# Kernel tuning notes

Hardware: AMD Instinct MI355X
Metric: run time of the kernel (lower is better)

The kernel has to match this reference:

```python
import jax, jax.numpy as jnp
import numpy as np

G = 17  # groups == deform_groups
EPS = 1e-5

# regular 3x3 kernel grid in homogeneous coords: rows = (dy, dx, 1), cols = 9 kernel taps (row-major)
REG = jnp.array([[-1, -1, -1, 0, 0, 0, 1, 1, 1],
                 [-1, 0, 1, -1, 0, 1, -1, 0, 1],
                 [1, 1, 1, 1, 1, 1, 1, 1, 1]], dtype=jnp.float32)
KY = jnp.array([-1, -1, -1, 0, 0, 0, 1, 1, 1], dtype=jnp.float32)
KX = jnp.array([-1, 0, 1, -1, 0, 1, -1, 0, 1], dtype=jnp.float32)


def setup_inputs() -> dict:
    key = jax.random.key(0)
    k0, k1, k2 = jax.random.split(key, 3)
    B, C, H, W = 2, 272, 128, 128
    Cg = C // G
    x = jax.random.normal(k0, (B, C, H, W), jnp.float32)
    tm_w = jax.random.normal(k1, (6 * G, Cg, 3, 3), jnp.float32) * 0.02  # offset-transform conv weight
    tm_b = jnp.zeros((6 * G,), jnp.float32)
    dc_w = jax.random.normal(k2, (C, Cg, 3, 3), jnp.float32) * 0.05     # deform conv weight (no bias)
    gamma = jnp.ones((C,), jnp.float32)
    beta = jnp.zeros((C,), jnp.float32)
    return dict(x=x, tm_w=tm_w, tm_b=tm_b, dc_w=dc_w, gamma=gamma, beta=beta)


def _deform_sample(x, dy, dx):
    """Bilinear-sample x (B,C,H,W) at per-group offsets dy,dx (B,H,W,G,9).
    Returns (B,G,Cg,9,H,W). Zero padding outside the image (mmcv semantics)."""
    B, C, H, W = x.shape
    Cg = C // G
    hh = jnp.arange(H, dtype=x.dtype)[None, :, None, None, None]
    ww = jnp.arange(W, dtype=x.dtype)[None, None, :, None, None]
    py = hh + KY + dy  # (B,H,W,G,9)
    px = ww + KX + dx
    y0 = jnp.floor(py)
    x0 = jnp.floor(px)
    wy = py - y0
    wx = px - x0
    y0i = y0.astype(jnp.int32)
    x0i = x0.astype(jnp.int32)
    x_g = x.reshape(B, G, Cg, H * W)

    def corner(yi, xi, wgt):
        valid = (yi >= 0) & (yi < H) & (xi >= 0) & (xi < W)
        lin = jnp.clip(yi, 0, H - 1) * W + jnp.clip(xi, 0, W - 1)  # (B,H,W,G,9)
        lin = lin.transpose(0, 3, 4, 1, 2).reshape(B, G, 1, 9 * H * W)
        idx = jnp.broadcast_to(lin, (B, G, Cg, 9 * H * W))
        vals = jnp.take_along_axis(x_g, idx, axis=3).reshape(B, G, Cg, 9, H, W)
        w = (wgt * valid.astype(x.dtype)).transpose(0, 3, 4, 1, 2)  # (B,G,9,H,W)
        return vals * w[:, :, None]

    samp = corner(y0i, x0i, (1 - wy) * (1 - wx))
    samp = samp + corner(y0i, x0i + 1, (1 - wy) * wx)
    samp = samp + corner(y0i + 1, x0i, wy * (1 - wx))
    samp = samp + corner(y0i + 1, x0i + 1, wy * wx)
    return samp


def _forward(x, tm_w, tm_b, dc_w, gamma, beta):
    B, C, H, W = x.shape
    Cg = C // G
    # 1) offset-transform conv (grouped 3x3, SAME)
    aff = jax.lax.conv_general_dilated(
        x, tm_w, window_strides=(1, 1), padding='SAME',
        dimension_numbers=('NCHW', 'OIHW', 'NCHW'), feature_group_count=G)
    aff = aff + tm_b[None, :, None, None]  # (B,6G,H,W)
    # faithful to torch: view(B,2,3,G,H,W).permute(0,4,5,3,1,2) @ REG
    aff = aff.reshape(B, 2, 3, G, H, W).transpose(0, 4, 5, 3, 1, 2)  # (B,H,W,G,2,3)
    off = jnp.einsum('bhwgij,jk->bhwgik', aff, REG)  # (B,H,W,G,2,9)
    # DeformConv2d reads the flattened 18 channels as interleaved (dy,dx) pairs per tap
    off = off.reshape(B, H, W, G, 18).reshape(B, H, W, G, 9, 2)
    dy, dx = off[..., 0], off[..., 1]
    # 2) deformable 3x3 conv, groups=deform_groups=G, bias=False
    samp = _deform_sample(x, dy, dx)  # (B,G,Cg,9,H,W)
    w = dc_w.reshape(G, Cg, Cg, 3 * 3)  # (g, out-in-group, in-in-group, tap)
    out = jnp.einsum('bgckhw,gock->bgohw', samp, w).reshape(B, C, H, W)
    # 3) batch norm (training-mode stats) + residual ReLU
    mean = jnp.mean(out, axis=(0, 2, 3), keepdims=True)
    var = jnp.var(out, axis=(0, 2, 3), keepdims=True)
    out = (out - mean) * jax.lax.rsqrt(var + EPS)
    out = out * gamma[None, :, None, None] + beta[None, :, None, None]
    return jax.nn.relu(out + x)


def reference(x, tm_w, tm_b, dc_w, gamma, beta):
    return _forward(x, tm_w, tm_b, dc_w, gamma, beta)
```

## Files before the change

kernel.cpp:

```cpp
#include <hip/hip_runtime.h>
#include <math.h>

#define BB 2
#define CC 272
#define GG 17
#define CG 16
#define HH 128
#define WW 128
#define HWX (HH*WW)
#define AFFC 102
#define NSLAB (BB*GG)
#define TILES_PER_SLAB 128
#define NWG (NSLAB*TILES_PER_SLAB)
#define WGPX (NWG/8)
#define PSTR ((size_t)NSLAB*HWX*4)

typedef float f4nt __attribute__((ext_vector_type(4)));
typedef float f2nt __attribute__((ext_vector_type(2)));
typedef unsigned u4nt __attribute__((ext_vector_type(4)));
typedef _Float16 h2 __attribute__((ext_vector_type(2)));

__device__ __forceinline__ h2 bch(unsigned u) { return __builtin_bit_cast(h2, u); }
__device__ __forceinline__ unsigned hpk(float a, float b) {
    return __builtin_bit_cast(unsigned, __builtin_amdgcn_cvt_pkrtz(a, b));
}
__device__ __forceinline__ h2 hbc(float a) {
    return __builtin_bit_cast(h2, __builtin_amdgcn_cvt_pkrtz(a, a));
}

#if __has_builtin(__builtin_amdgcn_fdot2)
#define FDOT2(A, B, C) __builtin_amdgcn_fdot2((A), (B), (C), false)
#else
#define FDOT2(A, B, C) fmaf((float)(A).x, (float)(B).x, fmaf((float)(A).y, (float)(B).y, (C)))
#endif

__device__ __forceinline__ unsigned f2bf(float f) {
    unsigned u = __float_as_uint(f);
    return (u + 0x7fffu + ((u >> 16) & 1u)) >> 16;
}
__device__ __forceinline__ float bflo(unsigned u) { return __uint_as_float(u << 16); }
__device__ __forceinline__ float bfhi(unsigned u) { return __uint_as_float(u & 0xffff0000u); }

__global__ __launch_bounds__(256) void wt_kernel(
    const float* __restrict__ dc_w, const float* __restrict__ tm_w,
    unsigned* __restrict__ dc_wh, unsigned* __restrict__ tm_wh)
{
    int i = blockIdx.x * 256 + threadIdx.x;
    if (i < GG * 8 * 9 * CG) {
        int oc = i & 15, t = (i >> 4) % 9, cp = (i / 144) % 8, g = i / 1152;
        float w0 = dc_w[((size_t)(g * 16 + oc) * 16 + 2 * cp) * 9 + t];
        float w1 = dc_w[((size_t)(g * 16 + oc) * 16 + 2 * cp + 1) * 9 + t];
        dc_wh[i] = hpk(w0, w1);
    }
    if (i < GG * 6 * 9 * 8) {
        int cp = i & 7, t = (i >> 3) % 9, j = (i / 72) % 6, ig = i / 432;
        float w0 = tm_w[((size_t)(ig * 6 + j) * 16 + 2 * cp) * 9 + t];
        float w1 = tm_w[((size_t)(ig * 6 + j) * 16 + 2 * cp + 1) * 9 + t];
        tm_wh[i] = hpk(w0, w1);
    }
}

__global__ __launch_bounds__(256) void transpose_kernel(
    const float* __restrict__ x, unsigned* __restrict__ xt)
{
    __shared__ float tile[CG][WW + 1];
    const int h = blockIdx.x & (HH - 1);
    const int g = (blockIdx.x >> 7) % GG;
    const int b = blockIdx.x / (GG * HH);
    const int tid = threadIdx.x;
    const float* src = x + (size_t)(b * CC + g * CG) * HWX + h * WW;
    for (int i = tid; i < CG * WW; i += 256) {
        int c = i >> 7, w = i & (WW - 1);
        tile[c][w] = src[(size_t)c * HWX + w];
    }
    __syncthreads();
    const size_t rowbase = ((size_t)(b * GG + g) * HWX + h * WW) * 4;
    unsigned* d0 = xt + rowbase;
    unsigned* d1 = xt + PSTR + rowbase;
    for (int i = tid; i < 4 * WW; i += 256) {
        int w = i >> 2, c4 = i & 3;
        d0[(size_t)w * 4 + c4] = hpk(tile[2 * c4][w],     tile[2 * c4 + 1][w]);
        d1[(size_t)w * 4 + c4] = hpk(tile[8 + 2 * c4][w], tile[8 + 2 * c4 + 1][w]);
    }
}

__global__ __launch_bounds__(128) void aff_conv_kernel(
    const unsigned* __restrict__ xt, const unsigned* __restrict__ tm_wh,
    const float* __restrict__ tm_b, float* __restrict__ aff2)
{
    const int ig = blockIdx.y;
    const int b = blockIdx.z;
    const int tid = threadIdx.x;

    const int p = blockIdx.x * 128 + tid;
    const int h = p >> 7, w = p & (WW - 1);
    const unsigned* xb0 = xt + (size_t)(b * GG + ig) * HWX * 4;
    const unsigned* xb1 = xb0 + PSTR;
    const unsigned* wbh = tm_wh + (size_t)ig * (6 * 9 * 8);

    float acc[6];
#pragma unroll
    for (int j = 0; j < 6; ++j) acc[j] = 0.f;

#pragma unroll 1
    for (int t = 0; t < 9; ++t) {
        int hy = h + t / 3 - 1;
        int wx = w + t % 3 - 1;
        uint4 u0 = {0, 0, 0, 0}, u1 = {0, 0, 0, 0};
        if (hy >= 0 && hy < HH && wx >= 0 && wx < WW) {
            u0 = *(const uint4*)(xb0 + (size_t)(hy * WW + wx) * 4);
            u1 = *(const uint4*)(xb1 + (size_t)(hy * WW + wx) * 4);
        }
#pragma unroll
        for (int j = 0; j < 6; ++j) {
            const uint4* wp = (const uint4*)(wbh + (j * 9 + t) * 8);
            uint4 qa = wp[0], qb = wp[1];
            float a = acc[j];
            a = FDOT2(bch(u0.x), bch(qa.x), a); a = FDOT2(bch(u0.y), bch(qa.y), a);
            a = FDOT2(bch(u0.z), bch(qa.z), a); a = FDOT2(bch(u0.w), bch(qa.w), a);
            a = FDOT2(bch(u1.x), bch(qb.x), a); a = FDOT2(bch(u1.y), bch(qb.y), a);
            a = FDOT2(bch(u1.z), bch(qb.z), a); a = FDOT2(bch(u1.w), bch(qb.w), a);
            acc[j] = a;
        }
    }
#pragma unroll
    for (int j = 0; j < 6; ++j) {
        int o = ig * 6 + j;
        int i_ = o / 51, rem = o % 51;
        int j2 = rem / 17, gp = rem % 17;
        int e = i_ * 3 + j2;
        aff2[((size_t)(b * GG + gp) * HWX + p) * 6 + e] = acc[j] + tm_b[o];
    }
}


#define MACC(T, CP, S2) { \
    const uint4* wp_ = (const uint4*)(wgh + ((CP) * 9 + (T)) * CG); \
    uint4 q0 = wp_[0], q1 = wp_[1], q2 = wp_[2], q3 = wp_[3]; \
    acc[0]  = FDOT2(S2, bch(q0.x), acc[0]);  acc[1]  = FDOT2(S2, bch(q0.y), acc[1]); \
    acc[2]  = FDOT2(S2, bch(q0.z), acc[2]);  acc[3]  = FDOT2(S2, bch(q0.w), acc[3]); \
    acc[4]  = FDOT2(S2, bch(q1.x), acc[4]);  acc[5]  = FDOT2(S2, bch(q1.y), acc[5]); \
    acc[6]  = FDOT2(S2, bch(q1.z), acc[6]);  acc[7]  = FDOT2(S2, bch(q1.w), acc[7]); \
    acc[8]  = FDOT2(S2, bch(q2.x), acc[8]);  acc[9]  = FDOT2(S2, bch(q2.y), acc[9]); \
    acc[10] = FDOT2(S2, bch(q2.z), acc[10]); acc[11] = FDOT2(S2, bch(q2.w), acc[11]); \
    acc[12] = FDOT2(S2, bch(q3.x), acc[12]); acc[13] = FDOT2(S2, bch(q3.y), acc[13]); \
    acc[14] = FDOT2(S2, bch(q3.z), acc[14]); acc[15] = FDOT2(S2, bch(q3.w), acc[15]); }

#define SEM(T, CP, UA, UB, UC, UD) { \
    h2 s2 = bch(UA) * W00 + bch(UB) * W01 + bch(UC) * W10 + bch(UD) * W11; \
    MACC(T, CP, s2) }

#define TAP(T, I0, K0, I1, K1) { \
    float dy = ((I0) ? a10 : a00) * (float)((K0) / 3 - 1) \
             + ((I0) ? a11 : a01) * (float)((K0) % 3 - 1) + ((I0) ? a12 : a02); \
    float dx = ((I1) ? a10 : a00) * (float)((K1) / 3 - 1) \
             + ((I1) ? a11 : a01) * (float)((K1) % 3 - 1) + ((I1) ? a12 : a02); \
    float py = (float)(h + (T) / 3 - 1) + dy; \
    float px = (float)(w + (T) % 3 - 1) + dx; \
    float y0f = floorf(py), x0f = floorf(px); \
    float wy = py - y0f, wx = px - x0f; \
    int y0 = (int)y0f, x0 = (int)x0f; \
    int y1 = y0 + 1, x1 = x0 + 1; \
    bool vy0 = (y0 >= 0) && (y0 < HH), vy1 = (y1 >= 0) && (y1 < HH); \
    bool vx0 = (x0 >= 0) && (x0 < WW), vx1 = (x1 >= 0) && (x1 < WW); \
    int y0c = min(max(y0, 0), HH - 1), y1c = min(max(y1, 0), HH - 1); \
    int x0c = min(max(x0, 0), WW - 1), x1c = min(max(x1, 0), WW - 1); \
    float w00 = (vy0 && vx0) ? (1.f - wy) * (1.f - wx) : 0.f; \
    float w01 = (vy0 && vx1) ? (1.f - wy) * wx : 0.f; \
    float w10 = (vy1 && vx0) ? wy * (1.f - wx) : 0.f; \
    float w11 = (vy1 && vx1) ? wy * wx : 0.f; \
    h2 W00 = hbc(w00), W01 = hbc(w01), W10 = hbc(w10), W11 = hbc(w11); \
    int l00 = y0c * WW + x0c, l01 = y0c * WW + x1c; \
    int l10 = y1c * WW + x0c, l11 = y1c * WW + x1c; \
    uint4 A0 = *(const uint4*)(xb0 + (size_t)l00 * 4); \
    uint4 A1 = *(const uint4*)(xb1 + (size_t)l00 * 4); \
    uint4 B0 = *(const uint4*)(xb0 + (size_t)l01 * 4); \
    uint4 B1 = *(const uint4*)(xb1 + (size_t)l01 * 4); \
    uint4 C0 = *(const uint4*)(xb0 + (size_t)l10 * 4); \
    uint4 C1 = *(const uint4*)(xb1 + (size_t)l10 * 4); \
    uint4 D0 = *(const uint4*)(xb0 + (size_t)l11 * 4); \
    uint4 D1 = *(const uint4*)(xb1 + (size_t)l11 * 4); \
    SEM(T, 0, A0.x, B0.x, C0.x, D0.x) SEM(T, 1, A0.y, B0.y, C0.y, D0.y) \
    SEM(T, 2, A0.z, B0.z, C0.z, D0.z) SEM(T, 3, A0.w, B0.w, C0.w, D0.w) \
    SEM(T, 4, A1.x, B1.x, C1.x, D1.x) SEM(T, 5, A1.y, B1.y, C1.y, D1.y) \
    SEM(T, 6, A1.z, B1.z, C1.z, D1.z) SEM(T, 7, A1.w, B1.w, C1.w, D1.w) }

__global__ __launch_bounds__(128, 6) void deform_kernel(
    const unsigned* __restrict__ xt, const unsigned* __restrict__ dc_wh,
    const float* __restrict__ aff2, unsigned* __restrict__ pre,
    float* __restrict__ stat_sum, float* __restrict__ stat_sqs)
{
    __shared__ float red[CG][2][2];

    const int bid = blockIdx.x;
    const int work = (bid & 7) * WGPX + (bid >> 3);
    const int slab = work / TILES_PER_SLAB;
    const int tile = work % TILES_PER_SLAB;
    const int b = slab / GG;
    const int g = slab % GG;

    const int tid = threadIdx.y * 16 + threadIdx.x;
    const int h = (tile >> 3) * 8 + threadIdx.y;
    const int w = (tile & 7) * 16 + threadIdx.x;

    const float* ap = aff2 + ((size_t)(b * GG + g) * HWX + h * WW + w) * 6;
    f2nt v0 = __builtin_nontemporal_load((const f2nt*)ap);
    f2nt v1 = __builtin_nontemporal_load((const f2nt*)(ap + 2));
    f2nt v2 = __builtin_nontemporal_load((const f2nt*)(ap + 4));
    float a00 = v0.x, a01 = v0.y, a02 = v1.x;
    float a10 = v1.y, a11 = v2.x, a12 = v2.y;

    const unsigned* xb0 = xt + (size_t)(b * GG + g) * HWX * 4;
    const unsigned* xb1 = xb0 + PSTR;
    const unsigned* wgh = dc_wh + (size_t)g * (8 * 9 * CG);

    float acc[CG];
#pragma unroll
    for (int oc = 0; oc < CG; ++oc) acc[oc] = 0.f;

    TAP(0, 0, 0, 0, 1)
    TAP(1, 0, 2, 0, 3)
    TAP(2, 0, 4, 0, 5)
    TAP(3, 0, 6, 0, 7)
    TAP(4, 0, 8, 1, 0)
    TAP(5, 1, 1, 1, 2)
    TAP(6, 1, 3, 1, 4)
    TAP(7, 1, 5, 1, 6)
    TAP(8, 1, 7, 1, 8)

    unsigned pk[8];
#pragma unroll
    for (int k = 0; k < 8; ++k)
        pk[k] = f2bf(acc[2 * k]) | (f2bf(acc[2 * k + 1]) << 16);
    {
        u4nt q0 = {pk[0], pk[1], pk[2], pk[3]};
        u4nt q1 = {pk[4], pk[5], pk[6], pk[7]};
        u4nt* pp = (u4nt*)(pre + ((size_t)slab * HWX + h * WW + w) * (CG / 2));
        __builtin_nontemporal_store(q0, pp);
        __builtin_nontemporal_store(q1, pp + 1);
    }

    const int lane = tid & 63, wave = tid >> 6;
#pragma unroll
    for (int oc = 0; oc < CG; ++oc) {
        float s = acc[oc], q = acc[oc] * acc[oc];
#pragma unroll
        for (int off = 32; off > 0; off >>= 1) {
            s += __shfl_down(s, off);
            q += __shfl_down(q, off);
        }
        if (lane == 0) { red[oc][wave][0] = s; red[oc][wave][1] = q; }
    }
    __syncthreads();
    if (tid < CG) {
        float s = red[tid][0][0] + red[tid][1][0];
        float q = red[tid][0][1] + red[tid][1][1];
        int ch = g * CG + tid;
        atomicAdd(&stat_sum[ch], s);
        atomicAdd(&stat_sqs[ch], q);
    }
}

__global__ __launch_bounds__(128) void bn_res_relu_kernel(
    const unsigned* __restrict__ pre, const float* __restrict__ x,
    const float* __restrict__ ssum, const float* __restrict__ ssqs,
    const float* __restrict__ gamma, const float* __restrict__ beta,
    float* __restrict__ out)
{
    const int blk = blockIdx.x;
    const int slab = blk >> 5;
    const int chunk = blk & 31;
    const int b = slab / GG, g = slab % GG;
    const int px0 = chunk * 512 + threadIdx.x * 4;

    const float n = (float)(BB * HWX);
    float sc[16], sh[16];
#pragma unroll
    for (int oc = 0; oc < 16; ++oc) {
        int ch = g * CG + oc;
        float mean = ssum[ch] / n;
        float var = ssqs[ch] / n - mean * mean;
        float s = rsqrtf(var + 1e-5f) * gamma[ch];
        sc[oc] = s;
        sh[oc] = fmaf(-mean, s, beta[ch]);
    }

    const uint4* pp = (const uint4*)(pre + ((size_t)slab * HWX + px0) * (CG / 2));
    unsigned Pu[32];
#pragma unroll
    for (int k = 0; k < 8; ++k) {
        uint4 v = pp[k];
        Pu[4 * k] = v.x; Pu[4 * k + 1] = v.y; Pu[4 * k + 2] = v.z; Pu[4 * k + 3] = v.w;
    }
    const float* xb = x + (size_t)(b * CC + g * CG) * HWX + px0;
    float* ob = out + (size_t)(b * CC + g * CG) * HWX + px0;

#pragma unroll
    for (int oc = 0; oc < 16; ++oc) {
        f4nt xv = __builtin_nontemporal_load((const f4nt*)(xb + (size_t)oc * HWX));
        f4nt r;
        float p0, p1, p2, p3;
        {
            unsigned u0 = Pu[0 * 8 + (oc >> 1)], u1 = Pu[1 * 8 + (oc >> 1)];
            unsigned u2 = Pu[2 * 8 + (oc >> 1)], u3 = Pu[3 * 8 + (oc >> 1)];
            p0 = (oc & 1) ? bfhi(u0) : bflo(u0);
            p1 = (oc & 1) ? bfhi(u1) : bflo(u1);
            p2 = (oc & 1) ? bfhi(u2) : bflo(u2);
            p3 = (oc & 1) ? bfhi(u3) : bflo(u3);
        }
        r.x = fmaxf(fmaf(p0, sc[oc], sh[oc]) + xv.x, 0.f);
        r.y = fmaxf(fmaf(p1, sc[oc], sh[oc]) + xv.y, 0.f);
        r.z = fmaxf(fmaf(p2, sc[oc], sh[oc]) + xv.z, 0.f);
        r.w = fmaxf(fmaf(p3, sc[oc], sh[oc]) + xv.w, 0.f);
        __builtin_nontemporal_store(r, (f4nt*)(ob + (size_t)oc * HWX));
    }
}

extern "C" void kernel_launch(void* const* d_in, const int* in_sizes, int n_in,
                              void* d_out, int out_size, void* d_ws, size_t ws_size,
                              hipStream_t stream)
{
    const float* x     = (const float*)d_in[0];
    const float* tm_w  = (const float*)d_in[1];
    const float* tm_b  = (const float*)d_in[2];
    const float* dc_w  = (const float*)d_in[3];
    const float* gamma = (const float*)d_in[4];
    const float* beta  = (const float*)d_in[5];
    float* out = (float*)d_out;

    float* ws = (float*)d_ws;
    float* stat_sum = ws;
    float* stat_sqs = ws + CC;
    unsigned* dc_wh = (unsigned*)(ws + 2048);
    unsigned* tm_wh = dc_wh + 19712;
    float* aff2 = (float*)(tm_wh + 7424);
    unsigned* xtb = (unsigned*)(aff2 + (size_t)BB * GG * HWX * 6);
    unsigned* preb = xtb + 2 * PSTR;

    (void)hipMemsetAsync(stat_sum, 0, 2 * CC * sizeof(float), stream);

    wt_kernel<<<dim3(77), dim3(256), 0, stream>>>(dc_w, tm_w, dc_wh, tm_wh);
    transpose_kernel<<<dim3(BB * GG * HH), dim3(256), 0, stream>>>(x, xtb);
    aff_conv_kernel<<<dim3(HWX / 128, GG, BB), dim3(128), 0, stream>>>(xtb, tm_wh, tm_b, aff2);
    deform_kernel<<<dim3(NWG), dim3(16, 8), 0, stream>>>(
        xtb, dc_wh, aff2, preb, stat_sum, stat_sqs);
    bn_res_relu_kernel<<<dim3(NSLAB * 32), dim3(128), 0, stream>>>(
        preb, x, stat_sum, stat_sqs, gamma, beta, out);
}
```

Baseline: 120.2 us.

## Software-pipeline deform tap gathers with double-buffered registers

Splits each tap into a load phase (offset math, bilinear weights, eight 16-byte gathers) and a multiply-accumulate phase. Two register buffer sets alternate so tap t+1's gathers are in flight while tap t's dot products run. Launch bounds drop from 6 to 4 waves per SIMD to leave room for the extra live registers. This trades occupancy-based latency hiding for explicit instruction-level overlap.

```diff
diff --git a/kernel.cpp b/kernel.cpp
--- a/kernel.cpp
+++ b/kernel.cpp
@@ -146,11 +146,11 @@
     acc[12] = FDOT2(S2, bch(q3.x), acc[12]); acc[13] = FDOT2(S2, bch(q3.y), acc[13]); \
     acc[14] = FDOT2(S2, bch(q3.z), acc[14]); acc[15] = FDOT2(S2, bch(q3.w), acc[15]); }
 
-#define SEM(T, CP, UA, UB, UC, UD) { \
-    h2 s2 = bch(UA) * W00 + bch(UB) * W01 + bch(UC) * W10 + bch(UD) * W11; \
+#define SEMS(T, CP, UA, UB, UC, UD, S) { \
+    h2 s2 = bch(UA) * W00##S + bch(UB) * W01##S + bch(UC) * W10##S + bch(UD) * W11##S; \
     MACC(T, CP, s2) }
 
-#define TAP(T, I0, K0, I1, K1) { \
+#define TAPLOAD(T, I0, K0, I1, K1, S) { \
     float dy = ((I0) ? a10 : a00) * (float)((K0) / 3 - 1) \
              + ((I0) ? a11 : a01) * (float)((K0) % 3 - 1) + ((I0) ? a12 : a02); \
     float dx = ((I1) ? a10 : a00) * (float)((K1) / 3 - 1) \
@@ -169,23 +169,29 @@
     float w01 = (vy0 && vx1) ? (1.f - wy) * wx : 0.f; \
     float w10 = (vy1 && vx0) ? wy * (1.f - wx) : 0.f; \
     float w11 = (vy1 && vx1) ? wy * wx : 0.f; \
-    h2 W00 = hbc(w00), W01 = hbc(w01), W10 = hbc(w10), W11 = hbc(w11); \
+    W00##S = hbc(w00); W01##S = hbc(w01); W10##S = hbc(w10); W11##S = hbc(w11); \
     int l00 = y0c * WW + x0c, l01 = y0c * WW + x1c; \
     int l10 = y1c * WW + x0c, l11 = y1c * WW + x1c; \
-    uint4 A0 = *(const uint4*)(xb0 + (size_t)l00 * 4); \
-    uint4 A1 = *(const uint4*)(xb1 + (size_t)l00 * 4); \
-    uint4 B0 = *(const uint4*)(xb0 + (size_t)l01 * 4); \
-    uint4 B1 = *(const uint4*)(xb1 + (size_t)l01 * 4); \
-    uint4 C0 = *(const uint4*)(xb0 + (size_t)l10 * 4); \
-    uint4 C1 = *(const uint4*)(xb1 + (size_t)l10 * 4); \
-    uint4 D0 = *(const uint4*)(xb0 + (size_t)l11 * 4); \
-    uint4 D1 = *(const uint4*)(xb1 + (size_t)l11 * 4); \
-    SEM(T, 0, A0.x, B0.x, C0.x, D0.x) SEM(T, 1, A0.y, B0.y, C0.y, D0.y) \
-    SEM(T, 2, A0.z, B0.z, C0.z, D0.z) SEM(T, 3, A0.w, B0.w, C0.w, D0.w) \
-    SEM(T, 4, A1.x, B1.x, C1.x, D1.x) SEM(T, 5, A1.y, B1.y, C1.y, D1.y) \
-    SEM(T, 6, A1.z, B1.z, C1.z, D1.z) SEM(T, 7, A1.w, B1.w, C1.w, D1.w) }
-
-__global__ __launch_bounds__(128, 6) void deform_kernel(
+    A0##S = *(const uint4*)(xb0 + (size_t)l00 * 4); \
+    A1##S = *(const uint4*)(xb1 + (size_t)l00 * 4); \
+    B0##S = *(const uint4*)(xb0 + (size_t)l01 * 4); \
+    B1##S = *(const uint4*)(xb1 + (size_t)l01 * 4); \
+    C0##S = *(const uint4*)(xb0 + (size_t)l10 * 4); \
+    C1##S = *(const uint4*)(xb1 + (size_t)l10 * 4); \
+    D0##S = *(const uint4*)(xb0 + (size_t)l11 * 4); \
+    D1##S = *(const uint4*)(xb1 + (size_t)l11 * 4); }
+
+#define TAPMAC(T, S) \
+    SEMS(T, 0, A0##S.x, B0##S.x, C0##S.x, D0##S.x, S) \
+    SEMS(T, 1, A0##S.y, B0##S.y, C0##S.y, D0##S.y, S) \
+    SEMS(T, 2, A0##S.z, B0##S.z, C0##S.z, D0##S.z, S) \
+    SEMS(T, 3, A0##S.w, B0##S.w, C0##S.w, D0##S.w, S) \
+    SEMS(T, 4, A1##S.x, B1##S.x, C1##S.x, D1##S.x, S) \
+    SEMS(T, 5, A1##S.y, B1##S.y, C1##S.y, D1##S.y, S) \
+    SEMS(T, 6, A1##S.z, B1##S.z, C1##S.z, D1##S.z, S) \
+    SEMS(T, 7, A1##S.w, B1##S.w, C1##S.w, D1##S.w, S)
+
+__global__ __launch_bounds__(128, 4) void deform_kernel(
     const unsigned* __restrict__ xt, const unsigned* __restrict__ dc_wh,
     const float* __restrict__ aff2, unsigned* __restrict__ pre,
     float* __restrict__ stat_sum, float* __restrict__ stat_sqs)
@@ -218,15 +224,20 @@
 #pragma unroll
     for (int oc = 0; oc < CG; ++oc) acc[oc] = 0.f;
 
-    TAP(0, 0, 0, 0, 1)
-    TAP(1, 0, 2, 0, 3)
-    TAP(2, 0, 4, 0, 5)
-    TAP(3, 0, 6, 0, 7)
-    TAP(4, 0, 8, 1, 0)
-    TAP(5, 1, 1, 1, 2)
-    TAP(6, 1, 3, 1, 4)
-    TAP(7, 1, 5, 1, 6)
-    TAP(8, 1, 7, 1, 8)
+    h2 W00a, W01a, W10a, W11a, W00b, W01b, W10b, W11b;
+    uint4 A0a, A1a, B0a, B1a, C0a, C1a, D0a, D1a;
+    uint4 A0b, A1b, B0b, B1b, C0b, C1b, D0b, D1b;
+
+    TAPLOAD(0, 0, 0, 0, 1, a)
+    TAPLOAD(1, 0, 2, 0, 3, b)  TAPMAC(0, a)
+    TAPLOAD(2, 0, 4, 0, 5, a)  TAPMAC(1, b)
+    TAPLOAD(3, 0, 6, 0, 7, b)  TAPMAC(2, a)
+    TAPLOAD(4, 0, 8, 1, 0, a)  TAPMAC(3, b)
+    TAPLOAD(5, 1, 1, 1, 2, b)  TAPMAC(4, a)
+    TAPLOAD(6, 1, 3, 1, 4, a)  TAPMAC(5, b)
+    TAPLOAD(7, 1, 5, 1, 6, b)  TAPMAC(6, a)
+    TAPLOAD(8, 1, 7, 1, 8, a)  TAPMAC(7, b)
+    TAPMAC(8, a)
 
     unsigned pk[8];
 #pragma unroll
```

Result: slower. 155.0 us (+29.0%).
